# Optimization experiments

Measured on AMD Instinct MI355X. Metric: run time of the kernel, lower is better.

Reference implementation:

```python
import jax, jax.numpy as jnp
import numpy as np

N = 262144
MUL0, MUL1, MUL2 = 128, 64, 32          # multiplicities of 0e, 1o, 2e
D0, D1, D2 = MUL0, MUL1 * 3, MUL2 * 5   # flat dims: 128, 192, 160
NG = MUL1 + MUL2                        # 96 gate scalars (0e)
NS = MUL0 + NG                          # 224 scalar outputs of the Linear


def _norm2mom_cst(f):
    # e3nn normalize2mom: rescale activation so E_{x~N(0,1)}[f(x)^2] = 1
    xs = np.random.default_rng(0).standard_normal(1_000_000).astype(np.float32)
    return float(1.0 / np.sqrt(np.mean(np.asarray(f(jnp.asarray(xs))) ** 2)))

CST_SILU = _norm2mom_cst(jax.nn.silu)
CST_RELU = _norm2mom_cst(jax.nn.relu)


def setup_inputs() -> dict:
    key = jax.random.key(0)
    k = jax.random.split(key, 5)
    return {
        "x": jax.random.normal(k[0], (N, D0 + D1 + D2), jnp.float32),
        "W0": jax.random.normal(k[1], (MUL0, NS), jnp.float32),
        "b0": jax.random.normal(k[2], (NS,), jnp.float32),
        "W1": jax.random.normal(k[3], (MUL1, MUL1), jnp.float32),
        "W2": jax.random.normal(k[4], (MUL2, MUL2), jnp.float32),
    }


def reference(x, W0, b0, W1, W2):
    n = x.shape[0]
    # split input into irrep blocks: [n,128] 0e, [n,64,3] 1o, [n,32,5] 2e
    x0 = x[:, :D0]
    x1 = x[:, D0:D0 + D1].reshape(n, MUL1, 3)
    x2 = x[:, D0 + D1:].reshape(n, MUL2, 5)
    # e3nn o3.Linear: per-irrep block matmul with 1/sqrt(fan_in) path norm;
    # bias only on scalar (0e) outputs
    s = x0 @ W0 * (1.0 / np.sqrt(MUL0)) + b0                      # [n,224]
    v = jnp.einsum('nim,ij->njm', x1, W1) * (1.0 / np.sqrt(MUL1))  # [n,64,3]
    t = jnp.einsum('nim,ij->njm', x2, W2) * (1.0 / np.sqrt(MUL2))  # [n,32,5]
    # e3nn Gate: silu on the 128 true scalars, relu on the 96 gates,
    # gated irreps multiplied channelwise by their gate scalar
    scalars = CST_SILU * jax.nn.silu(s[:, :MUL0])                  # [n,128]
    gates = CST_RELU * jax.nn.relu(s[:, MUL0:])                    # [n,96]
    gv = (v * gates[:, :MUL1, None]).reshape(n, D1)                # [n,192]
    gt = (t * gates[:, MUL1:, None]).reshape(n, D2)                # [n,160]
    return jnp.concatenate([scalars, gv, gt], axis=-1)            # [n,480]
```

## Files before the change

### kernel.cpp

```cpp
#include <hip/hip_runtime.h>
#include <hip/hip_bf16.h>

#define NROWS   262144
#define DIN     480
#define DOUT    480

#define M_TILE  32
#define XSTR    488

#define CST_SILU 1.6765290f
#define CST_RELU 1.4142135623730951f
#define INV_S128 0.08838834764831845f
#define INV_S64  0.125f
#define INV_S32  0.17677669529663687f

#define WS_FRAGS 66
#define WS_BYTES (WS_FRAGS * 64 * 16)

typedef short bf16x8 __attribute__((ext_vector_type(8)));
typedef float f32x4  __attribute__((ext_vector_type(4)));

__device__ __forceinline__ ushort f2bf(float f) {
    unsigned u = __float_as_uint(f);
    u = (u + 0x7FFFu + ((u >> 16) & 1u)) >> 16;
    return (ushort)u;
}

__device__ __forceinline__ unsigned pk2(float a, float b) {
    __hip_bfloat162 h = __float22bfloat162_rn(float2{a, b});
    return *reinterpret_cast<unsigned*>(&h);
}

__device__ __forceinline__ bf16x8 load_b_frag(const float* __restrict__ W, int ldw,
                                              int kbase, int nbase, int lane) {
    int n  = nbase + (lane & 15);
    int k0 = kbase + ((lane >> 4) << 3);
    bf16x8 f;
#pragma unroll
    for (int e = 0; e < 8; ++e) f[e] = (short)f2bf(W[(k0 + e) * ldw + n]);
    return f;
}

__global__ __launch_bounds__(64) void prep_frags(
        const float* __restrict__ W0, const float* __restrict__ W1,
        const float* __restrict__ W2, ushort* __restrict__ ws) {
    const int b = blockIdx.x, lane = threadIdx.x;
    const int lr = lane & 15, kg = lane >> 4;
    const float* W; int ldw, n, k0;
    if (b < 56)      { W = W0; ldw = 224; n = (b >> 2) * 16 + lr; k0 = (b & 3) * 32 + (kg << 3); }
    else if (b < 64) { int t = b - 56; W = W1; ldw = 64; n = (t >> 1) * 16 + lr; k0 = (t & 1) * 32 + (kg << 3); }
    else             { W = W2; ldw = 32; n = (b - 64) * 16 + lr; k0 = (kg << 3); }
    bf16x8 f;
#pragma unroll
    for (int e = 0; e < 8; ++e) f[e] = (short)f2bf(W[(k0 + e) * ldw + n]);
    *reinterpret_cast<bf16x8*>(ws + (b * 64 + lane) * 8) = f;
}

template <bool PRE>
__global__ __launch_bounds__(256, 5) void percep_kernel(
        const float* __restrict__ x,  const float* __restrict__ W0,
        const float* __restrict__ bias0, const float* __restrict__ W1,
        const float* __restrict__ W2, float* __restrict__ out,
        const ushort* __restrict__ ws) {
    __shared__ __align__(16) ushort xs[M_TILE * XSTR];

    const int tid  = threadIdx.x;
    const int lane = tid & 63;
    const int wid  = tid >> 6;
    const int lr   = lane & 15;
    const int kg   = lane >> 4;
    const int rf   = wid >> 1;
    const int half = wid & 1;
    const int row0 = blockIdx.x * M_TILE;
    const bf16x8* F = reinterpret_cast<const bf16x8*>(ws);

#pragma unroll
    for (int it = 0; it < 4; ++it) {
        int idx = tid + it * 256;
        int row = idx >> 5, c4 = idx & 31;
        const float4 v = reinterpret_cast<const float4*>(x + (row0 + row) * DIN)[c4];
        uint2 o = { pk2(v.x, v.y), pk2(v.z, v.w) };
        *reinterpret_cast<uint2*>(&xs[row * XSTR + c4 * 4]) = o;
    }
#pragma unroll
    for (int it = 0; it < 2; ++it) {
        int idx = tid + it * 256;
        int row = idx >> 4, g = idx & 15;
        const float4* p = reinterpret_cast<const float4*>(x + (row0 + row) * DIN + 128 + 12 * g);
        float4 q0 = p[0], q1 = p[1], q2 = p[2];
        float v[12] = { q0.x, q0.y, q0.z, q0.w, q1.x, q1.y, q1.z, q1.w, q2.x, q2.y, q2.z, q2.w };
#pragma unroll
        for (int m = 0; m < 3; ++m) {
            uint2 o = { pk2(v[m], v[m + 3]), pk2(v[m + 6], v[m + 9]) };
            *reinterpret_cast<uint2*>(&xs[row * XSTR + 128 + 64 * m + 4 * g]) = o;
        }
    }
    {
        int row = tid >> 3, g = tid & 7;
        const float4* p = reinterpret_cast<const float4*>(x + (row0 + row) * DIN + 320 + 20 * g);
        float4 q0 = p[0], q1 = p[1], q2 = p[2], q3 = p[3], q4 = p[4];
        float v[20] = { q0.x, q0.y, q0.z, q0.w, q1.x, q1.y, q1.z, q1.w, q2.x, q2.y, q2.z, q2.w,
                        q3.x, q3.y, q3.z, q3.w, q4.x, q4.y, q4.z, q4.w };
#pragma unroll
        for (int m = 0; m < 5; ++m) {
            uint2 o = { pk2(v[m], v[m + 5]), pk2(v[m + 10], v[m + 15]) };
            *reinterpret_cast<uint2*>(&xs[row * XSTR + 320 + 32 * m + 4 * g]) = o;
        }
    }
    __syncthreads();

    bf16x8 aS[4];
#pragma unroll
    for (int kk = 0; kk < 4; ++kk)
        aS[kk] = *reinterpret_cast<const bf16x8*>(
            &xs[(rf * 16 + lr) * XSTR + kk * 32 + (kg << 3)]);

    const int orow = row0 + rf * 16 + (kg << 2);

    auto s_acc = [&](int st) -> f32x4 {
        f32x4 acc = { 0.f, 0.f, 0.f, 0.f };
#pragma unroll
        for (int kk = 0; kk < 4; ++kk) {
            bf16x8 b = PRE ? F[(st * 4 + kk) * 64 + lane]
                           : load_b_frag(W0, 224, kk * 32, st * 16, lane);
            acc = __builtin_amdgcn_mfma_f32_16x16x32_bf16(aS[kk], b, acc, 0, 0, 0);
        }
        return acc;
    };
    auto gate_tile = [&](int st) -> f32x4 {
        f32x4 acc = s_acc(st);
        float bias = bias0[st * 16 + lr];
        f32x4 g;
#pragma unroll
        for (int r = 0; r < 4; ++r) {
            float s = acc[r] * INV_S128 + bias;
            g[r] = fmaxf(s, 0.f) * CST_RELU;
        }
        return g;
    };
    auto silu_tile = [&](int st) {
        f32x4 acc = s_acc(st);
        float bias = bias0[st * 16 + lr];
#pragma unroll
        for (int r = 0; r < 4; ++r) {
            float s = acc[r] * INV_S128 + bias;
            float val = CST_SILU * s * __builtin_amdgcn_rcpf(1.f + __expf(-s));
            out[(orow + r) * DOUT + st * 16 + lr] = val;
        }
    };
    auto v_tile = [&](int jtg, f32x4 g) {
        f32x4 a0 = {0,0,0,0}, a1 = {0,0,0,0}, a2 = {0,0,0,0};
#pragma unroll
        for (int kk = 0; kk < 2; ++kk) {
            bf16x8 b = PRE ? F[(56 + jtg * 2 + kk) * 64 + lane]
                           : load_b_frag(W1, 64, kk * 32, jtg * 16, lane);
            const ushort* base = &xs[(rf * 16 + lr) * XSTR + 128 + kk * 32 + (kg << 3)];
            a0 = __builtin_amdgcn_mfma_f32_16x16x32_bf16(*reinterpret_cast<const bf16x8*>(base +   0), b, a0, 0, 0, 0);
            a1 = __builtin_amdgcn_mfma_f32_16x16x32_bf16(*reinterpret_cast<const bf16x8*>(base +  64), b, a1, 0, 0, 0);
            a2 = __builtin_amdgcn_mfma_f32_16x16x32_bf16(*reinterpret_cast<const bf16x8*>(base + 128), b, a2, 0, 0, 0);
        }
        int j = jtg * 16 + lr;
#pragma unroll
        for (int r = 0; r < 4; ++r) {
            float gg = g[r] * INV_S64;
            float* po = out + (orow + r) * DOUT + 128 + 3 * j;
            po[0] = a0[r] * gg; po[1] = a1[r] * gg; po[2] = a2[r] * gg;
        }
    };
    auto t_tile = [&](int tu, f32x4 g) {
        bf16x8 bt = PRE ? F[(64 + tu) * 64 + lane]
                        : load_b_frag(W2, 32, 0, tu * 16, lane);
        const ushort* base = &xs[(rf * 16 + lr) * XSTR + 320 + (kg << 3)];
        f32x4 z = {0,0,0,0};
        f32x4 a0 = __builtin_amdgcn_mfma_f32_16x16x32_bf16(*reinterpret_cast<const bf16x8*>(base +   0), bt, z, 0, 0, 0);
        f32x4 a1 = __builtin_amdgcn_mfma_f32_16x16x32_bf16(*reinterpret_cast<const bf16x8*>(base +  32), bt, z, 0, 0, 0);
        f32x4 a2 = __builtin_amdgcn_mfma_f32_16x16x32_bf16(*reinterpret_cast<const bf16x8*>(base +  64), bt, z, 0, 0, 0);
        f32x4 a3 = __builtin_amdgcn_mfma_f32_16x16x32_bf16(*reinterpret_cast<const bf16x8*>(base +  96), bt, z, 0, 0, 0);
        f32x4 a4 = __builtin_amdgcn_mfma_f32_16x16x32_bf16(*reinterpret_cast<const bf16x8*>(base + 128), bt, z, 0, 0, 0);
        int j = tu * 16 + lr;
#pragma unroll
        for (int r = 0; r < 4; ++r) {
            float gg = g[r] * INV_S32;
            float* po = out + (orow + r) * DOUT + 320 + 5 * j;
            po[0] = a0[r] * gg; po[1] = a1[r] * gg; po[2] = a2[r] * gg;
            po[3] = a3[r] * gg; po[4] = a4[r] * gg;
        }
    };

    const int gt0 = half ? 10 : 8, gt1 = half ? 11 : 9, gt2 = half ? 13 : 12;
    {
        f32x4 g0 = gate_tile(gt0);
        v_tile(half * 2 + 0, g0);
    }
    silu_tile(half * 4 + 0);
    {
        f32x4 g1 = gate_tile(gt1);
        v_tile(half * 2 + 1, g1);
    }
    silu_tile(half * 4 + 1);
    {
        f32x4 g2 = gate_tile(gt2);
        t_tile(half, g2);
    }
    silu_tile(half * 4 + 2);
    silu_tile(half * 4 + 3);
}

extern "C" void kernel_launch(void* const* d_in, const int* in_sizes, int n_in,
                              void* d_out, int out_size, void* d_ws, size_t ws_size,
                              hipStream_t stream) {
    const float* x  = (const float*)d_in[0];
    const float* W0 = (const float*)d_in[1];
    const float* b0 = (const float*)d_in[2];
    const float* W1 = (const float*)d_in[3];
    const float* W2 = (const float*)d_in[4];
    float* out = (float*)d_out;
    dim3 grid(NROWS / M_TILE), block(256);
    if (ws_size >= WS_BYTES) {
        hipLaunchKernelGGL(prep_frags, dim3(WS_FRAGS), dim3(64), 0, stream, W0, W1, W2, (ushort*)d_ws);
        hipLaunchKernelGGL((percep_kernel<true>), grid, block, 0, stream,
                           x, W0, b0, W1, W2, out, (const ushort*)d_ws);
    } else {
        hipLaunchKernelGGL((percep_kernel<false>), grid, block, 0, stream,
                           x, W0, b0, W1, W2, out, (const ushort*)d_ws);
    }
}
```

Before: 243.5 us.

## Halve row tile to 16 with two-wave blocks and reorder gate computation

Shrinks each block to 16 rows and 128 threads, so each of two waves covers half the output columns for all rows of the tile. The three gate tiles and all silu tiles are now computed before the vector and tensor gated matmuls, instead of being interleaved. The aim is to halve LDS per block and launch twice as many blocks to improve latency hiding for this memory-bound kernel. The cost is more gate registers held live at once and per-block overhead that is no longer amortised.

```diff
diff --git a/kernel.cpp b/kernel.cpp
--- a/kernel.cpp
+++ b/kernel.cpp
@@ -5,7 +5,7 @@
 #define DIN     480
 #define DOUT    480
 
-#define M_TILE  32
+#define M_TILE  16
 #define XSTR    488
 
 #define CST_SILU 1.6765290f
@@ -57,7 +57,7 @@
 }
 
 template <bool PRE>
-__global__ __launch_bounds__(256, 5) void percep_kernel(
+__global__ __launch_bounds__(128, 4) void percep_kernel(
         const float* __restrict__ x,  const float* __restrict__ W0,
         const float* __restrict__ bias0, const float* __restrict__ W1,
         const float* __restrict__ W2, float* __restrict__ out,
@@ -66,17 +66,15 @@
 
     const int tid  = threadIdx.x;
     const int lane = tid & 63;
-    const int wid  = tid >> 6;
+    const int w    = tid >> 6;
     const int lr   = lane & 15;
     const int kg   = lane >> 4;
-    const int rf   = wid >> 1;
-    const int half = wid & 1;
     const int row0 = blockIdx.x * M_TILE;
     const bf16x8* F = reinterpret_cast<const bf16x8*>(ws);
 
 #pragma unroll
     for (int it = 0; it < 4; ++it) {
-        int idx = tid + it * 256;
+        int idx = tid + it * 128;
         int row = idx >> 5, c4 = idx & 31;
         const float4 v = reinterpret_cast<const float4*>(x + (row0 + row) * DIN)[c4];
         uint2 o = { pk2(v.x, v.y), pk2(v.z, v.w) };
@@ -84,7 +82,7 @@
     }
 #pragma unroll
     for (int it = 0; it < 2; ++it) {
-        int idx = tid + it * 256;
+        int idx = tid + it * 128;
         int row = idx >> 4, g = idx & 15;
         const float4* p = reinterpret_cast<const float4*>(x + (row0 + row) * DIN + 128 + 12 * g);
         float4 q0 = p[0], q1 = p[1], q2 = p[2];
@@ -112,10 +110,9 @@
     bf16x8 aS[4];
 #pragma unroll
     for (int kk = 0; kk < 4; ++kk)
-        aS[kk] = *reinterpret_cast<const bf16x8*>(
-            &xs[(rf * 16 + lr) * XSTR + kk * 32 + (kg << 3)]);
-
-    const int orow = row0 + rf * 16 + (kg << 2);
+        aS[kk] = *reinterpret_cast<const bf16x8*>(&xs[lr * XSTR + kk * 32 + (kg << 3)]);
+
+    const int orow = row0 + (kg << 2);
 
     auto s_acc = [&](int st) -> f32x4 {
         f32x4 acc = { 0.f, 0.f, 0.f, 0.f };
@@ -148,62 +145,57 @@
             out[(orow + r) * DOUT + st * 16 + lr] = val;
         }
     };
-    auto v_tile = [&](int jtg, f32x4 g) {
+
+    f32x4 gV0 = gate_tile(w ? 10 : 8);
+    f32x4 gV1 = gate_tile(w ? 11 : 9);
+    f32x4 gT  = gate_tile(w ? 13 : 12);
+    silu_tile(w * 4 + 0);
+    silu_tile(w * 4 + 1);
+    silu_tile(w * 4 + 2);
+    silu_tile(w * 4 + 3);
+
+#pragma unroll
+    for (int jt = 0; jt < 2; ++jt) {
+        const int jtg = w * 2 + jt;
         f32x4 a0 = {0,0,0,0}, a1 = {0,0,0,0}, a2 = {0,0,0,0};
 #pragma unroll
         for (int kk = 0; kk < 2; ++kk) {
             bf16x8 b = PRE ? F[(56 + jtg * 2 + kk) * 64 + lane]
                            : load_b_frag(W1, 64, kk * 32, jtg * 16, lane);
-            const ushort* base = &xs[(rf * 16 + lr) * XSTR + 128 + kk * 32 + (kg << 3)];
+            const ushort* base = &xs[lr * XSTR + 128 + kk * 32 + (kg << 3)];
             a0 = __builtin_amdgcn_mfma_f32_16x16x32_bf16(*reinterpret_cast<const bf16x8*>(base +   0), b, a0, 0, 0, 0);
             a1 = __builtin_amdgcn_mfma_f32_16x16x32_bf16(*reinterpret_cast<const bf16x8*>(base +  64), b, a1, 0, 0, 0);
             a2 = __builtin_amdgcn_mfma_f32_16x16x32_bf16(*reinterpret_cast<const bf16x8*>(base + 128), b, a2, 0, 0, 0);
         }
+        const f32x4& gv = jt ? gV1 : gV0;
         int j = jtg * 16 + lr;
 #pragma unroll
         for (int r = 0; r < 4; ++r) {
-            float gg = g[r] * INV_S64;
+            float gg = gv[r] * INV_S64;
             float* po = out + (orow + r) * DOUT + 128 + 3 * j;
             po[0] = a0[r] * gg; po[1] = a1[r] * gg; po[2] = a2[r] * gg;
         }
-    };
-    auto t_tile = [&](int tu, f32x4 g) {
-        bf16x8 bt = PRE ? F[(64 + tu) * 64 + lane]
-                        : load_b_frag(W2, 32, 0, tu * 16, lane);
-        const ushort* base = &xs[(rf * 16 + lr) * XSTR + 320 + (kg << 3)];
+    }
+
+    {
+        bf16x8 bt = PRE ? F[(64 + w) * 64 + lane]
+                        : load_b_frag(W2, 32, 0, w * 16, lane);
+        const ushort* base = &xs[lr * XSTR + 320 + (kg << 3)];
         f32x4 z = {0,0,0,0};
         f32x4 a0 = __builtin_amdgcn_mfma_f32_16x16x32_bf16(*reinterpret_cast<const bf16x8*>(base +   0), bt, z, 0, 0, 0);
         f32x4 a1 = __builtin_amdgcn_mfma_f32_16x16x32_bf16(*reinterpret_cast<const bf16x8*>(base +  32), bt, z, 0, 0, 0);
         f32x4 a2 = __builtin_amdgcn_mfma_f32_16x16x32_bf16(*reinterpret_cast<const bf16x8*>(base +  64), bt, z, 0, 0, 0);
         f32x4 a3 = __builtin_amdgcn_mfma_f32_16x16x32_bf16(*reinterpret_cast<const bf16x8*>(base +  96), bt, z, 0, 0, 0);
         f32x4 a4 = __builtin_amdgcn_mfma_f32_16x16x32_bf16(*reinterpret_cast<const bf16x8*>(base + 128), bt, z, 0, 0, 0);
-        int j = tu * 16 + lr;
-#pragma unroll
-        for (int r = 0; r < 4; ++r) {
-            float gg = g[r] * INV_S32;
+        int j = w * 16 + lr;
+#pragma unroll
+        for (int r = 0; r < 4; ++r) {
+            float gg = gT[r] * INV_S32;
             float* po = out + (orow + r) * DOUT + 320 + 5 * j;
             po[0] = a0[r] * gg; po[1] = a1[r] * gg; po[2] = a2[r] * gg;
             po[3] = a3[r] * gg; po[4] = a4[r] * gg;
         }
-    };
-
-    const int gt0 = half ? 10 : 8, gt1 = half ? 11 : 9, gt2 = half ? 13 : 12;
-    {
-        f32x4 g0 = gate_tile(gt0);
-        v_tile(half * 2 + 0, g0);
-    }
-    silu_tile(half * 4 + 0);
-    {
-        f32x4 g1 = gate_tile(gt1);
-        v_tile(half * 2 + 1, g1);
-    }
-    silu_tile(half * 4 + 1);
-    {
-        f32x4 g2 = gate_tile(gt2);
-        t_tile(half, g2);
-    }
-    silu_tile(half * 4 + 2);
-    silu_tile(half * 4 + 3);
+    }
 }
 
 extern "C" void kernel_launch(void* const* d_in, const int* in_sizes, int n_in,
@@ -215,7 +207,7 @@
     const float* W1 = (const float*)d_in[3];
     const float* W2 = (const float*)d_in[4];
     float* out = (float*)d_out;
-    dim3 grid(NROWS / M_TILE), block(256);
+    dim3 grid(NROWS / M_TILE), block(128);
     if (ws_size >= WS_BYTES) {
         hipLaunchKernelGGL(prep_frags, dim3(WS_FRAGS), dim3(64), 0, stream, W0, W1, W2, (ushort*)d_ws);
         hipLaunchKernelGGL((percep_kernel<true>), grid, block, 0, stream,
```

After: 236.7 us. 2.8% less time.

## Make blocks persistent with a producer warp double-buffering input tiles

Applied to the files above, without the earlier changes.

Each block now processes 16 row tiles instead of one. A dedicated producer wavefront loads and converts the next tile into a second LDS buffer while the other three wavefronts compute the current tile. Work is also repartitioned: two compute waves handle the vector gates and one handles the tensor gates plus silu. The aim is to overlap global loads with MFMA and epilogue work and to cut block launch overhead. The cost is that only one wave issues loads, which may limit memory-level parallelism, and the three compute waves carry uneven loads. Occupancy is also lower (2 blocks/CU) and the grid is small.

```diff
diff --git a/kernel.cpp b/kernel.cpp
--- a/kernel.cpp
+++ b/kernel.cpp
@@ -6,6 +6,8 @@
 #define DOUT    480
 
 #define M_TILE  32
+#define TILES   16
+#define GRIDSZ  (NROWS / (M_TILE * TILES))
 #define XSTR    488
 
 #define CST_SILU 1.6765290f
@@ -25,7 +27,6 @@
     u = (u + 0x7FFFu + ((u >> 16) & 1u)) >> 16;
     return (ushort)u;
 }
-
 __device__ __forceinline__ unsigned pk2(float a, float b) {
     __hip_bfloat162 h = __float22bfloat162_rn(float2{a, b});
     return *reinterpret_cast<unsigned*>(&h);
@@ -57,153 +58,191 @@
 }
 
 template <bool PRE>
-__global__ __launch_bounds__(256, 5) void percep_kernel(
+__global__ __launch_bounds__(256, 2) void percep_kernel(
         const float* __restrict__ x,  const float* __restrict__ W0,
         const float* __restrict__ bias0, const float* __restrict__ W1,
         const float* __restrict__ W2, float* __restrict__ out,
         const ushort* __restrict__ ws) {
-    __shared__ __align__(16) ushort xs[M_TILE * XSTR];
+    __shared__ __align__(16) ushort xs[2][M_TILE * XSTR];
 
     const int tid  = threadIdx.x;
     const int lane = tid & 63;
     const int wid  = tid >> 6;
     const int lr   = lane & 15;
     const int kg   = lane >> 4;
-    const int rf   = wid >> 1;
-    const int half = wid & 1;
-    const int row0 = blockIdx.x * M_TILE;
+    const int blk_row0 = blockIdx.x * (M_TILE * TILES);
     const bf16x8* F = reinterpret_cast<const bf16x8*>(ws);
 
-#pragma unroll
-    for (int it = 0; it < 4; ++it) {
-        int idx = tid + it * 256;
-        int row = idx >> 5, c4 = idx & 31;
-        const float4 v = reinterpret_cast<const float4*>(x + (row0 + row) * DIN)[c4];
-        uint2 o = { pk2(v.x, v.y), pk2(v.z, v.w) };
-        *reinterpret_cast<uint2*>(&xs[row * XSTR + c4 * 4]) = o;
-    }
-#pragma unroll
-    for (int it = 0; it < 2; ++it) {
-        int idx = tid + it * 256;
-        int row = idx >> 4, g = idx & 15;
-        const float4* p = reinterpret_cast<const float4*>(x + (row0 + row) * DIN + 128 + 12 * g);
-        float4 q0 = p[0], q1 = p[1], q2 = p[2];
-        float v[12] = { q0.x, q0.y, q0.z, q0.w, q1.x, q1.y, q1.z, q1.w, q2.x, q2.y, q2.z, q2.w };
-#pragma unroll
-        for (int m = 0; m < 3; ++m) {
-            uint2 o = { pk2(v[m], v[m + 3]), pk2(v[m + 6], v[m + 9]) };
-            *reinterpret_cast<uint2*>(&xs[row * XSTR + 128 + 64 * m + 4 * g]) = o;
-        }
-    }
-    {
-        int row = tid >> 3, g = tid & 7;
-        const float4* p = reinterpret_cast<const float4*>(x + (row0 + row) * DIN + 320 + 20 * g);
-        float4 q0 = p[0], q1 = p[1], q2 = p[2], q3 = p[3], q4 = p[4];
-        float v[20] = { q0.x, q0.y, q0.z, q0.w, q1.x, q1.y, q1.z, q1.w, q2.x, q2.y, q2.z, q2.w,
-                        q3.x, q3.y, q3.z, q3.w, q4.x, q4.y, q4.z, q4.w };
-#pragma unroll
-        for (int m = 0; m < 5; ++m) {
-            uint2 o = { pk2(v[m], v[m + 5]), pk2(v[m + 10], v[m + 15]) };
-            *reinterpret_cast<uint2*>(&xs[row * XSTR + 320 + 32 * m + 4 * g]) = o;
-        }
-    }
-    __syncthreads();
-
-    bf16x8 aS[4];
-#pragma unroll
-    for (int kk = 0; kk < 4; ++kk)
-        aS[kk] = *reinterpret_cast<const bf16x8*>(
-            &xs[(rf * 16 + lr) * XSTR + kk * 32 + (kg << 3)]);
-
-    const int orow = row0 + rf * 16 + (kg << 2);
-
-    auto s_acc = [&](int st) -> f32x4 {
-        f32x4 acc = { 0.f, 0.f, 0.f, 0.f };
-#pragma unroll
-        for (int kk = 0; kk < 4; ++kk) {
-            bf16x8 b = PRE ? F[(st * 4 + kk) * 64 + lane]
-                           : load_b_frag(W0, 224, kk * 32, st * 16, lane);
-            acc = __builtin_amdgcn_mfma_f32_16x16x32_bf16(aS[kk], b, acc, 0, 0, 0);
-        }
-        return acc;
-    };
-    auto gate_tile = [&](int st) -> f32x4 {
-        f32x4 acc = s_acc(st);
-        float bias = bias0[st * 16 + lr];
-        f32x4 g;
-#pragma unroll
-        for (int r = 0; r < 4; ++r) {
-            float s = acc[r] * INV_S128 + bias;
-            g[r] = fmaxf(s, 0.f) * CST_RELU;
-        }
-        return g;
-    };
-    auto silu_tile = [&](int st) {
-        f32x4 acc = s_acc(st);
-        float bias = bias0[st * 16 + lr];
-#pragma unroll
-        for (int r = 0; r < 4; ++r) {
-            float s = acc[r] * INV_S128 + bias;
-            float val = CST_SILU * s * __builtin_amdgcn_rcpf(1.f + __expf(-s));
-            out[(orow + r) * DOUT + st * 16 + lr] = val;
+    auto stage = [&](int buf, int row0) {
+        ushort* bb = xs[buf];
+#pragma unroll 1
+        for (int sub = 0; sub < 4; ++sub) {
+            const int vt = (sub << 6) + lane;
+            const int rA = vt >> 5, cA = vt & 31;
+            const int rB = vt >> 4, gB = vt & 15;
+            const int rC = vt >> 3, gC = vt & 7;
+            float4 a0, a1, a2, a3, b0, b1, b2, b3, b4, b5, c0, c1, c2, c3, c4;
+            a0 = reinterpret_cast<const float4*>(x + (row0 + rA     ) * DIN)[cA];
+            a1 = reinterpret_cast<const float4*>(x + (row0 + rA +  8) * DIN)[cA];
+            a2 = reinterpret_cast<const float4*>(x + (row0 + rA + 16) * DIN)[cA];
+            a3 = reinterpret_cast<const float4*>(x + (row0 + rA + 24) * DIN)[cA];
+            { const float4* p = reinterpret_cast<const float4*>(x + (row0 + rB) * DIN + 128 + 12 * gB);
+              b0 = p[0]; b1 = p[1]; b2 = p[2]; }
+            { const float4* p = reinterpret_cast<const float4*>(x + (row0 + rB + 16) * DIN + 128 + 12 * gB);
+              b3 = p[0]; b4 = p[1]; b5 = p[2]; }
+            { const float4* p = reinterpret_cast<const float4*>(x + (row0 + rC) * DIN + 320 + 20 * gC);
+              c0 = p[0]; c1 = p[1]; c2 = p[2]; c3 = p[3]; c4 = p[4]; }
+
+            { uint2 o = { pk2(a0.x, a0.y), pk2(a0.z, a0.w) };
+              *reinterpret_cast<uint2*>(&bb[(rA     ) * XSTR + cA * 4]) = o; }
+            { uint2 o = { pk2(a1.x, a1.y), pk2(a1.z, a1.w) };
+              *reinterpret_cast<uint2*>(&bb[(rA +  8) * XSTR + cA * 4]) = o; }
+            { uint2 o = { pk2(a2.x, a2.y), pk2(a2.z, a2.w) };
+              *reinterpret_cast<uint2*>(&bb[(rA + 16) * XSTR + cA * 4]) = o; }
+            { uint2 o = { pk2(a3.x, a3.y), pk2(a3.z, a3.w) };
+              *reinterpret_cast<uint2*>(&bb[(rA + 24) * XSTR + cA * 4]) = o; }
+            { float v[12] = { b0.x, b0.y, b0.z, b0.w, b1.x, b1.y, b1.z, b1.w, b2.x, b2.y, b2.z, b2.w };
+#pragma unroll
+              for (int m = 0; m < 3; ++m) {
+                  uint2 o = { pk2(v[m], v[m + 3]), pk2(v[m + 6], v[m + 9]) };
+                  *reinterpret_cast<uint2*>(&bb[rB * XSTR + 128 + 64 * m + 4 * gB]) = o;
+              } }
+            { float v[12] = { b3.x, b3.y, b3.z, b3.w, b4.x, b4.y, b4.z, b4.w, b5.x, b5.y, b5.z, b5.w };
+#pragma unroll
+              for (int m = 0; m < 3; ++m) {
+                  uint2 o = { pk2(v[m], v[m + 3]), pk2(v[m + 6], v[m + 9]) };
+                  *reinterpret_cast<uint2*>(&bb[(rB + 16) * XSTR + 128 + 64 * m + 4 * gB]) = o;
+              } }
+            { float v[20] = { c0.x, c0.y, c0.z, c0.w, c1.x, c1.y, c1.z, c1.w, c2.x, c2.y, c2.z, c2.w,
+                              c3.x, c3.y, c3.z, c3.w, c4.x, c4.y, c4.z, c4.w };
+#pragma unroll
+              for (int m = 0; m < 5; ++m) {
+                  uint2 o = { pk2(v[m], v[m + 5]), pk2(v[m + 10], v[m + 15]) };
+                  *reinterpret_cast<uint2*>(&bb[rC * XSTR + 320 + 32 * m + 4 * gC]) = o;
+              } }
         }
     };
-    auto v_tile = [&](int jtg, f32x4 g) {
-        f32x4 a0 = {0,0,0,0}, a1 = {0,0,0,0}, a2 = {0,0,0,0};
-#pragma unroll
-        for (int kk = 0; kk < 2; ++kk) {
-            bf16x8 b = PRE ? F[(56 + jtg * 2 + kk) * 64 + lane]
-                           : load_b_frag(W1, 64, kk * 32, jtg * 16, lane);
-            const ushort* base = &xs[(rf * 16 + lr) * XSTR + 128 + kk * 32 + (kg << 3)];
-            a0 = __builtin_amdgcn_mfma_f32_16x16x32_bf16(*reinterpret_cast<const bf16x8*>(base +   0), b, a0, 0, 0, 0);
-            a1 = __builtin_amdgcn_mfma_f32_16x16x32_bf16(*reinterpret_cast<const bf16x8*>(base +  64), b, a1, 0, 0, 0);
-            a2 = __builtin_amdgcn_mfma_f32_16x16x32_bf16(*reinterpret_cast<const bf16x8*>(base + 128), b, a2, 0, 0, 0);
-        }
-        int j = jtg * 16 + lr;
-#pragma unroll
-        for (int r = 0; r < 4; ++r) {
-            float gg = g[r] * INV_S64;
-            float* po = out + (orow + r) * DOUT + 128 + 3 * j;
-            po[0] = a0[r] * gg; po[1] = a1[r] * gg; po[2] = a2[r] * gg;
+
+    auto compute = [&](int buf, int row0) {
+        const ushort* bb = xs[buf];
+        bf16x8 aS[2][4];
+#pragma unroll
+        for (int rf = 0; rf < 2; ++rf)
+#pragma unroll
+            for (int kk = 0; kk < 4; ++kk)
+                aS[rf][kk] = *reinterpret_cast<const bf16x8*>(
+                    &bb[(rf * 16 + lr) * XSTR + kk * 32 + (kg << 3)]);
+
+        auto s_acc = [&](int st, int rf) -> f32x4 {
+            f32x4 acc = { 0.f, 0.f, 0.f, 0.f };
+#pragma unroll
+            for (int kk = 0; kk < 4; ++kk) {
+                bf16x8 b = PRE ? F[(st * 4 + kk) * 64 + lane]
+                               : load_b_frag(W0, 224, kk * 32, st * 16, lane);
+                acc = __builtin_amdgcn_mfma_f32_16x16x32_bf16(aS[rf][kk], b, acc, 0, 0, 0);
+            }
+            return acc;
+        };
+        auto gate_tile = [&](int st, int rf) -> f32x4 {
+            f32x4 acc = s_acc(st, rf);
+            float bias = bias0[st * 16 + lr];
+            f32x4 g;
+#pragma unroll
+            for (int r = 0; r < 4; ++r) {
+                float s = acc[r] * INV_S128 + bias;
+                g[r] = fmaxf(s, 0.f) * CST_RELU;
+            }
+            return g;
+        };
+        auto silu_tile = [&](int st, int rf) {
+            f32x4 acc = s_acc(st, rf);
+            float bias = bias0[st * 16 + lr];
+            int orow = row0 + rf * 16 + (kg << 2);
+#pragma unroll
+            for (int r = 0; r < 4; ++r) {
+                float s = acc[r] * INV_S128 + bias;
+                float val = CST_SILU * s * __builtin_amdgcn_rcpf(1.f + __expf(-s));
+                out[(orow + r) * DOUT + st * 16 + lr] = val;
+            }
+        };
+        auto v_tile = [&](int jtg, int rf, f32x4 g) {
+            f32x4 a0 = {0,0,0,0}, a1 = {0,0,0,0}, a2 = {0,0,0,0};
+#pragma unroll
+            for (int kk = 0; kk < 2; ++kk) {
+                bf16x8 b = PRE ? F[(56 + jtg * 2 + kk) * 64 + lane]
+                               : load_b_frag(W1, 64, kk * 32, jtg * 16, lane);
+                const ushort* base = &bb[(rf * 16 + lr) * XSTR + 128 + kk * 32 + (kg << 3)];
+                a0 = __builtin_amdgcn_mfma_f32_16x16x32_bf16(*reinterpret_cast<const bf16x8*>(base +   0), b, a0, 0, 0, 0);
+                a1 = __builtin_amdgcn_mfma_f32_16x16x32_bf16(*reinterpret_cast<const bf16x8*>(base +  64), b, a1, 0, 0, 0);
+                a2 = __builtin_amdgcn_mfma_f32_16x16x32_bf16(*reinterpret_cast<const bf16x8*>(base + 128), b, a2, 0, 0, 0);
+            }
+            int j = jtg * 16 + lr;
+            int orow = row0 + rf * 16 + (kg << 2);
+#pragma unroll
+            for (int r = 0; r < 4; ++r) {
+                float gg = g[r] * INV_S64;
+                float* po = out + (orow + r) * DOUT + 128 + 3 * j;
+                po[0] = a0[r] * gg; po[1] = a1[r] * gg; po[2] = a2[r] * gg;
+            }
+        };
+        auto t_tile = [&](int tu, int rf, f32x4 g) {
+            bf16x8 bt = PRE ? F[(64 + tu) * 64 + lane]
+                            : load_b_frag(W2, 32, 0, tu * 16, lane);
+            const ushort* base = &bb[(rf * 16 + lr) * XSTR + 320 + (kg << 3)];
+            f32x4 z = {0,0,0,0};
+            f32x4 a0 = __builtin_amdgcn_mfma_f32_16x16x32_bf16(*reinterpret_cast<const bf16x8*>(base +   0), bt, z, 0, 0, 0);
+            f32x4 a1 = __builtin_amdgcn_mfma_f32_16x16x32_bf16(*reinterpret_cast<const bf16x8*>(base +  32), bt, z, 0, 0, 0);
+            f32x4 a2 = __builtin_amdgcn_mfma_f32_16x16x32_bf16(*reinterpret_cast<const bf16x8*>(base +  64), bt, z, 0, 0, 0);
+            f32x4 a3 = __builtin_amdgcn_mfma_f32_16x16x32_bf16(*reinterpret_cast<const bf16x8*>(base +  96), bt, z, 0, 0, 0);
+            f32x4 a4 = __builtin_amdgcn_mfma_f32_16x16x32_bf16(*reinterpret_cast<const bf16x8*>(base + 128), bt, z, 0, 0, 0);
+            int j = tu * 16 + lr;
+            int orow = row0 + rf * 16 + (kg << 2);
+#pragma unroll
+            for (int r = 0; r < 4; ++r) {
+                float gg = g[r] * INV_S32;
+                float* po = out + (orow + r) * DOUT + 320 + 5 * j;
+                po[0] = a0[r] * gg; po[1] = a1[r] * gg; po[2] = a2[r] * gg;
+                po[3] = a3[r] * gg; po[4] = a4[r] * gg;
+            }
+        };
+
+        if (wid < 2) {
+            const int c = wid;
+#pragma unroll
+            for (int rf = 0; rf < 2; ++rf) { f32x4 g = gate_tile(8 + 2 * c, rf); v_tile(2 * c, rf, g); }
+#pragma unroll
+            for (int rf = 0; rf < 2; ++rf) silu_tile(2 * c, rf);
+#pragma unroll
+            for (int rf = 0; rf < 2; ++rf) { f32x4 g = gate_tile(9 + 2 * c, rf); v_tile(2 * c + 1, rf, g); }
+#pragma unroll
+            for (int rf = 0; rf < 2; ++rf) silu_tile(2 * c + 1, rf);
+        } else {
+#pragma unroll
+            for (int rf = 0; rf < 2; ++rf) { f32x4 g = gate_tile(12, rf); t_tile(0, rf, g); }
+#pragma unroll
+            for (int rf = 0; rf < 2; ++rf) silu_tile(4, rf);
+#pragma unroll
+            for (int rf = 0; rf < 2; ++rf) { f32x4 g = gate_tile(13, rf); t_tile(1, rf, g); }
+#pragma unroll
+            for (int rf = 0; rf < 2; ++rf) silu_tile(5, rf);
+#pragma unroll
+            for (int rf = 0; rf < 2; ++rf) silu_tile(6, rf);
+#pragma unroll
+            for (int rf = 0; rf < 2; ++rf) silu_tile(7, rf);
         }
     };
-    auto t_tile = [&](int tu, f32x4 g) {
-        bf16x8 bt = PRE ? F[(64 + tu) * 64 + lane]
-                        : load_b_frag(W2, 32, 0, tu * 16, lane);
-        const ushort* base = &xs[(rf * 16 + lr) * XSTR + 320 + (kg << 3)];
-        f32x4 z = {0,0,0,0};
-        f32x4 a0 = __builtin_amdgcn_mfma_f32_16x16x32_bf16(*reinterpret_cast<const bf16x8*>(base +   0), bt, z, 0, 0, 0);
-        f32x4 a1 = __builtin_amdgcn_mfma_f32_16x16x32_bf16(*reinterpret_cast<const bf16x8*>(base +  32), bt, z, 0, 0, 0);
-        f32x4 a2 = __builtin_amdgcn_mfma_f32_16x16x32_bf16(*reinterpret_cast<const bf16x8*>(base +  64), bt, z, 0, 0, 0);
-        f32x4 a3 = __builtin_amdgcn_mfma_f32_16x16x32_bf16(*reinterpret_cast<const bf16x8*>(base +  96), bt, z, 0, 0, 0);
-        f32x4 a4 = __builtin_amdgcn_mfma_f32_16x16x32_bf16(*reinterpret_cast<const bf16x8*>(base + 128), bt, z, 0, 0, 0);
-        int j = tu * 16 + lr;
-#pragma unroll
-        for (int r = 0; r < 4; ++r) {
-            float gg = g[r] * INV_S32;
-            float* po = out + (orow + r) * DOUT + 320 + 5 * j;
-            po[0] = a0[r] * gg; po[1] = a1[r] * gg; po[2] = a2[r] * gg;
-            po[3] = a3[r] * gg; po[4] = a4[r] * gg;
+
+    if (wid == 3) stage(0, blk_row0);
+    __syncthreads();
+#pragma unroll 1
+    for (int t = 0; t < TILES; ++t) {
+        if (wid == 3) {
+            if (t + 1 < TILES) stage((t + 1) & 1, blk_row0 + (t + 1) * M_TILE);
+        } else {
+            compute(t & 1, blk_row0 + t * M_TILE);
         }
-    };
-
-    const int gt0 = half ? 10 : 8, gt1 = half ? 11 : 9, gt2 = half ? 13 : 12;
-    {
-        f32x4 g0 = gate_tile(gt0);
-        v_tile(half * 2 + 0, g0);
+        __syncthreads();
     }
-    silu_tile(half * 4 + 0);
-    {
-        f32x4 g1 = gate_tile(gt1);
-        v_tile(half * 2 + 1, g1);
-    }
-    silu_tile(half * 4 + 1);
-    {
-        f32x4 g2 = gate_tile(gt2);
-        t_tile(half, g2);
-    }
-    silu_tile(half * 4 + 2);
-    silu_tile(half * 4 + 3);
 }
 
 extern "C" void kernel_launch(void* const* d_in, const int* in_sizes, int n_in,
@@ -215,7 +254,7 @@
     const float* W1 = (const float*)d_in[3];
     const float* W2 = (const float*)d_in[4];
     float* out = (float*)d_out;
-    dim3 grid(NROWS / M_TILE), block(256);
+    dim3 grid(GRIDSZ), block(256);
     if (ws_size >= WS_BYTES) {
         hipLaunchKernelGGL(prep_frags, dim3(WS_FRAGS), dim3(64), 0, stream, W0, W1, W2, (ushort*)d_ws);
         hipLaunchKernelGGL((percep_kernel<true>), grid, block, 0, stream,
```

Result: slower. 274.0 us (+12.5%).
